# Optimization experiments

Measured on AMD Instinct MI355X. Metric: run time of the kernel, lower is better.

The kernel has to match this reference:

```python
import jax, jax.numpy as jnp
import numpy as np

B, T, D, H = 256, 1024, 128, 128

def setup_inputs() -> dict:
    key = jax.random.key(0)
    k1, k2, k3, k4 = jax.random.split(key, 4)
    return {
        "x": jax.random.normal(k1, (B, T, D), dtype=jnp.float32),
        "w": jax.random.normal(k2, (D, H), dtype=jnp.float32) * 0.05,
        "state_weight": jax.random.normal(k3, (H, H), dtype=jnp.float32) * 0.05,
        "b": jax.random.normal(k4, (H,), dtype=jnp.float32) * 0.05,
    }

def reference(x, w, state_weight, b):
    # Faithful Elman RNN with return_sequences=False.
    # Original transposes input to time-major [T, B, D], initializes the
    # state from step 0 WITHOUT a recurrent term, then iterates steps 1..T-1.
    X = jnp.transpose(x, (1, 0, 2))  # [T, B, D]
    # Precompute input projections for all steps in one big GEMM (same math).
    proj = jnp.einsum("tbd,dh->tbh", X, w) + b  # [T, B, H]
    state0 = jnp.tanh(proj[0])

    def step(state, pt):
        y = jnp.tanh(pt + state @ state_weight)
        return y, None

    final_state, _ = jax.lax.scan(step, state0, proj[1:])
    return final_state  # [B, H]
```

## Files before the change

kernel.cpp:

```cpp
#include <hip/hip_runtime.h>

#define T_N 1024
#define H_N 128
#define CH   64
#define NCH (T_N / CH)
#define WPAD 136
#define PPAD 68
#define XGRP 1040
#define XBUF_BYTES (32 * XGRP)

typedef __attribute__((ext_vector_type(8))) short bf16x8;
typedef __attribute__((ext_vector_type(4))) float f32x4;

__device__ __forceinline__ short f2bf_rne(float f) {
    union { float f; unsigned int i; } v; v.f = f;
    unsigned int r = v.i + 0x7FFFu + ((v.i >> 16) & 1u);
    return (short)(r >> 16);
}
__device__ __forceinline__ float tanh_fast(float x) {
    return 1.0f - 2.0f / (__expf(2.0f * x) + 1.0f);
}

__global__ __launch_bounds__(256, 1) void k_fused(const float* __restrict__ x,
                                                  const float* __restrict__ w,
                                                  const float* __restrict__ wst,
                                                  const float* __restrict__ bias,
                                                  float* __restrict__ out) {
    __shared__ __align__(16) short wT[H_N * WPAD];
    __shared__ __align__(16) float pT[H_N * PPAD];
    __shared__ __align__(16) char  xbuf[2][XBUF_BYTES];
    __shared__ __align__(16) short sst[2][H_N];

    const int tid  = threadIdx.x;
    const int wv   = tid >> 6;
    const int lane = tid & 63;
    const int l = lane & 15;
    const int q = lane >> 4;
    const int r = blockIdx.x;
    const float* xrow = x + (size_t)r * T_N * H_N;
    const f32x4 zero4 = (f32x4){0.f, 0.f, 0.f, 0.f};

    {
        const char* gsrc = (const char*)xrow;
        #pragma unroll
        for (int kk = 0; kk < 8; ++kk) {
            int k = wv * 8 + kk;
            __builtin_amdgcn_global_load_lds(
                (const __attribute__((address_space(1))) void*)(gsrc + k * 1024 + lane * 16),
                (__attribute__((address_space(3))) void*)(&xbuf[0][k * XGRP]),
                16, 0, 0);
        }
    }

    short* wsT = reinterpret_cast<short*>(pT);
    for (int e = tid * 4; e < H_N * H_N; e += 1024) {
        int k = e >> 7, n = e & 127;
        float4 a4 = *reinterpret_cast<const float4*>(wst + e);
        wsT[(n + 0) * WPAD + k] = f2bf_rne(a4.x);
        wsT[(n + 1) * WPAD + k] = f2bf_rne(a4.y);
        wsT[(n + 2) * WPAD + k] = f2bf_rne(a4.z);
        wsT[(n + 3) * WPAD + k] = f2bf_rne(a4.w);
    }
    __syncthreads();

    bf16x8 wf[2][4];
    #pragma unroll
    for (int b = 0; b < 2; ++b)
        #pragma unroll
        for (int ks = 0; ks < 4; ++ks)
            wf[b][ks] = *reinterpret_cast<const bf16x8*>(
                &wsT[(16 * (2 * wv + b) + l) * WPAD + ks * 32 + q * 8]);

    for (int e = tid * 4; e < H_N * H_N; e += 1024) {
        int k = e >> 7, n = e & 127;
        float4 a4 = *reinterpret_cast<const float4*>(w + e);
        wT[(n + 0) * WPAD + k] = f2bf_rne(a4.x);
        wT[(n + 1) * WPAD + k] = f2bf_rne(a4.y);
        wT[(n + 2) * WPAD + k] = f2bf_rne(a4.z);
        wT[(n + 3) * WPAD + k] = f2bf_rne(a4.w);
    }

    float bv[8];
    #pragma unroll
    for (int nt = 0; nt < 8; ++nt) bv[nt] = bias[nt * 16 + l];

    int par = 0;
    float y0 = 0.f, y1 = 0.f;

    #pragma unroll 1
    for (int c = 0; c < NCH; ++c) {
        __syncthreads();

        {
            const char* xb = xbuf[c & 1];
            int row = wv * 16 + l;
            const float* pr = reinterpret_cast<const float*>(
                xb + (row >> 1) * XGRP + (row & 1) * 512);
            bf16x8 ax[4];
            #pragma unroll
            for (int ks = 0; ks < 4; ++ks) {
                float4 u0 = *reinterpret_cast<const float4*>(pr + ks * 32 + q * 8);
                float4 u1 = *reinterpret_cast<const float4*>(pr + ks * 32 + q * 8 + 4);
                bf16x8 f;
                f[0] = f2bf_rne(u0.x); f[1] = f2bf_rne(u0.y);
                f[2] = f2bf_rne(u0.z); f[3] = f2bf_rne(u0.w);
                f[4] = f2bf_rne(u1.x); f[5] = f2bf_rne(u1.y);
                f[6] = f2bf_rne(u1.z); f[7] = f2bf_rne(u1.w);
                ax[ks] = f;
            }
            #pragma unroll
            for (int nt = 0; nt < 8; ++nt) {
                f32x4 acc;
                #pragma unroll
                for (int ks = 0; ks < 4; ++ks) {
                    bf16x8 bw = *reinterpret_cast<const bf16x8*>(
                        &wT[(nt * 16 + l) * WPAD + ks * 32 + q * 8]);
                    acc = __builtin_amdgcn_mfma_f32_16x16x32_bf16(
                        ax[ks], bw, ks == 0 ? zero4 : acc, 0, 0, 0);
                }
                f32x4 o = (f32x4){acc[0] + bv[nt], acc[1] + bv[nt],
                                  acc[2] + bv[nt], acc[3] + bv[nt]};
                *reinterpret_cast<f32x4*>(&pT[(nt * 16 + l) * PPAD + wv * 16 + q * 4]) = o;
            }
        }

        if (c + 1 < NCH) {
            const char* gsrc = (const char*)(xrow + (size_t)(c + 1) * CH * H_N);
            char* ldst = &xbuf[(c + 1) & 1][0];
            #pragma unroll
            for (int kk = 0; kk < 8; ++kk) {
                int k = wv * 8 + kk;
                __builtin_amdgcn_global_load_lds(
                    (const __attribute__((address_space(1))) void*)(gsrc + k * 1024 + lane * 16),
                    (__attribute__((address_space(3))) void*)(ldst + k * XGRP),
                    16, 0, 0);
            }
        }

        __syncthreads();

        int tstart = 0;
        if (c == 0) {
            if (tid < 128) sst[0][tid] = f2bf_rne(tanh_fast(pT[tid * PPAD + 0]));
            __syncthreads();
            tstart = 1;
            par = 0;
        }

        float p0 = pT[(32 * wv + l) * PPAD + tstart];
        float p1 = pT[(32 * wv + 16 + l) * PPAD + tstart];

        #pragma unroll 1
        for (int t = tstart; t < CH; ++t) {
            bf16x8 a[4];
            #pragma unroll
            for (int ks = 0; ks < 4; ++ks)
                a[ks] = *reinterpret_cast<const bf16x8*>(&sst[par][ks * 32 + q * 8]);

            f32x4 acc[8];
            #pragma unroll
            for (int ks = 0; ks < 4; ++ks) {
                acc[ks]     = __builtin_amdgcn_mfma_f32_16x16x32_bf16(a[ks], wf[0][ks], zero4, 0, 0, 0);
                acc[4 + ks] = __builtin_amdgcn_mfma_f32_16x16x32_bf16(a[ks], wf[1][ks], zero4, 0, 0, 0);
            }

            int tn = (t + 1 < CH) ? t + 1 : t;
            float np0 = pT[(32 * wv + l) * PPAD + tn];
            float np1 = pT[(32 * wv + 16 + l) * PPAD + tn];

            float z0 = p0 + ((acc[0][0] + acc[1][0]) + (acc[2][0] + acc[3][0]));
            float z1 = p1 + ((acc[4][0] + acc[5][0]) + (acc[6][0] + acc[7][0]));
            y0 = tanh_fast(z0);
            y1 = tanh_fast(z1);
            sst[par ^ 1][32 * wv + l]      = f2bf_rne(y0);
            sst[par ^ 1][32 * wv + 16 + l] = f2bf_rne(y1);
            p0 = np0; p1 = np1;
            par ^= 1;
            __syncthreads();
        }
    }

    if (q == 0) {
        out[r * H_N + 32 * wv + l]      = y0;
        out[r * H_N + 32 * wv + 16 + l] = y1;
    }
}

extern "C" void kernel_launch(void* const* d_in, const int* in_sizes, int n_in,
                              void* d_out, int out_size, void* d_ws, size_t ws_size,
                              hipStream_t stream) {
    const float* x    = (const float*)d_in[0];
    const float* w    = (const float*)d_in[1];
    const float* wst  = (const float*)d_in[2];
    const float* bias = (const float*)d_in[3];
    float* out = (float*)d_out;

    k_fused<<<256, 256, 0, stream>>>(x, w, wst, bias, out);
}
```

Baseline: 464.4 us.

## Double chunk size, keep input weights in registers, pack state stores with permuted layout

Raises the time chunk from 64 to 128 steps and drops x double-buffering. The next chunk's x is now loaded into a single buffer after the projection finishes reading it, which halves the number of chunk transitions. The input projection weights are loaded once into registers, so each wave computes its own 32 output columns for all rows and the per-chunk LDS weight reads go away. The recurrent state is written as one packed 32-bit store per lane, using a permuted slot layout matched in the recurrent weights. Per-step __syncthreads are replaced with an lgkmcnt wait plus s_barrier. The risk is that x-load latency is no longer hidden behind the recurrence at chunk boundaries.

```diff
diff --git a/kernel.cpp b/kernel.cpp
--- a/kernel.cpp
+++ b/kernel.cpp
@@ -2,15 +2,16 @@
 
 #define T_N 1024
 #define H_N 128
-#define CH   64
+#define CH   128
 #define NCH (T_N / CH)
-#define WPAD 136
-#define PPAD 68
+#define SPAD 136
+#define PPAD 132
 #define XGRP 1040
-#define XBUF_BYTES (32 * XGRP)
 
 typedef __attribute__((ext_vector_type(8))) short bf16x8;
 typedef __attribute__((ext_vector_type(4))) float f32x4;
+
+#define BAR_LGKM() asm volatile("s_waitcnt lgkmcnt(0)\n\ts_barrier" ::: "memory")
 
 __device__ __forceinline__ short f2bf_rne(float f) {
     union { float f; unsigned int i; } v; v.f = f;
@@ -19,6 +20,9 @@
 }
 __device__ __forceinline__ float tanh_fast(float x) {
     return 1.0f - 2.0f / (__expf(2.0f * x) + 1.0f);
+}
+__device__ __forceinline__ int slotof(int c) {
+    return (c & 0x60) | ((c & 0x0F) << 1) | ((c >> 4) & 1);
 }
 
 __global__ __launch_bounds__(256, 1) void k_fused(const float* __restrict__ x,
@@ -26,9 +30,8 @@
                                                   const float* __restrict__ wst,
                                                   const float* __restrict__ bias,
                                                   float* __restrict__ out) {
-    __shared__ __align__(16) short wT[H_N * WPAD];
     __shared__ __align__(16) float pT[H_N * PPAD];
-    __shared__ __align__(16) char  xbuf[2][XBUF_BYTES];
+    __shared__ __align__(16) char  xbuf[64 * XGRP];
     __shared__ __align__(16) short sst[2][H_N];
 
     const int tid  = threadIdx.x;
@@ -43,46 +46,54 @@
     {
         const char* gsrc = (const char*)xrow;
         #pragma unroll
-        for (int kk = 0; kk < 8; ++kk) {
-            int k = wv * 8 + kk;
+        for (int kk = 0; kk < 16; ++kk) {
+            int k = wv * 16 + kk;
             __builtin_amdgcn_global_load_lds(
                 (const __attribute__((address_space(1))) void*)(gsrc + k * 1024 + lane * 16),
-                (__attribute__((address_space(3))) void*)(&xbuf[0][k * XGRP]),
+                (__attribute__((address_space(3))) void*)(&xbuf[k * XGRP]),
                 16, 0, 0);
         }
     }
 
-    short* wsT = reinterpret_cast<short*>(pT);
+    short* stg = reinterpret_cast<short*>(pT);
+
     for (int e = tid * 4; e < H_N * H_N; e += 1024) {
-        int k = e >> 7, n = e & 127;
+        int k = e >> 7, n = e & 127, s = slotof(k);
         float4 a4 = *reinterpret_cast<const float4*>(wst + e);
-        wsT[(n + 0) * WPAD + k] = f2bf_rne(a4.x);
-        wsT[(n + 1) * WPAD + k] = f2bf_rne(a4.y);
-        wsT[(n + 2) * WPAD + k] = f2bf_rne(a4.z);
-        wsT[(n + 3) * WPAD + k] = f2bf_rne(a4.w);
-    }
-    __syncthreads();
-
+        stg[(n + 0) * SPAD + s] = f2bf_rne(a4.x);
+        stg[(n + 1) * SPAD + s] = f2bf_rne(a4.y);
+        stg[(n + 2) * SPAD + s] = f2bf_rne(a4.z);
+        stg[(n + 3) * SPAD + s] = f2bf_rne(a4.w);
+    }
+    __syncthreads();
     bf16x8 wf[2][4];
     #pragma unroll
     for (int b = 0; b < 2; ++b)
         #pragma unroll
         for (int ks = 0; ks < 4; ++ks)
             wf[b][ks] = *reinterpret_cast<const bf16x8*>(
-                &wsT[(16 * (2 * wv + b) + l) * WPAD + ks * 32 + q * 8]);
+                &stg[(16 * (2 * wv + b) + l) * SPAD + ks * 32 + q * 8]);
+    __syncthreads();
 
     for (int e = tid * 4; e < H_N * H_N; e += 1024) {
         int k = e >> 7, n = e & 127;
         float4 a4 = *reinterpret_cast<const float4*>(w + e);
-        wT[(n + 0) * WPAD + k] = f2bf_rne(a4.x);
-        wT[(n + 1) * WPAD + k] = f2bf_rne(a4.y);
-        wT[(n + 2) * WPAD + k] = f2bf_rne(a4.z);
-        wT[(n + 3) * WPAD + k] = f2bf_rne(a4.w);
-    }
-
-    float bv[8];
+        stg[(n + 0) * SPAD + k] = f2bf_rne(a4.x);
+        stg[(n + 1) * SPAD + k] = f2bf_rne(a4.y);
+        stg[(n + 2) * SPAD + k] = f2bf_rne(a4.z);
+        stg[(n + 3) * SPAD + k] = f2bf_rne(a4.w);
+    }
+    __syncthreads();
+    bf16x8 wfin[2][4];
     #pragma unroll
-    for (int nt = 0; nt < 8; ++nt) bv[nt] = bias[nt * 16 + l];
+    for (int b = 0; b < 2; ++b)
+        #pragma unroll
+        for (int ks = 0; ks < 4; ++ks)
+            wfin[b][ks] = *reinterpret_cast<const bf16x8*>(
+                &stg[(16 * (2 * wv + b) + l) * SPAD + ks * 32 + q * 8]);
+    float bv0 = bias[16 * (2 * wv + 0) + l];
+    float bv1 = bias[16 * (2 * wv + 1) + l];
+    __syncthreads();
 
     int par = 0;
     float y0 = 0.f, y1 = 0.f;
@@ -91,11 +102,11 @@
     for (int c = 0; c < NCH; ++c) {
         __syncthreads();
 
-        {
-            const char* xb = xbuf[c & 1];
-            int row = wv * 16 + l;
+        #pragma unroll
+        for (int rt = 0; rt < 8; ++rt) {
+            int row = rt * 16 + l;
             const float* pr = reinterpret_cast<const float*>(
-                xb + (row >> 1) * XGRP + (row & 1) * 512);
+                xbuf + (row >> 1) * XGRP + (row & 1) * 512);
             bf16x8 ax[4];
             #pragma unroll
             for (int ks = 0; ks < 4; ++ks) {
@@ -109,40 +120,37 @@
                 ax[ks] = f;
             }
             #pragma unroll
-            for (int nt = 0; nt < 8; ++nt) {
+            for (int b = 0; b < 2; ++b) {
                 f32x4 acc;
                 #pragma unroll
-                for (int ks = 0; ks < 4; ++ks) {
-                    bf16x8 bw = *reinterpret_cast<const bf16x8*>(
-                        &wT[(nt * 16 + l) * WPAD + ks * 32 + q * 8]);
+                for (int ks = 0; ks < 4; ++ks)
                     acc = __builtin_amdgcn_mfma_f32_16x16x32_bf16(
-                        ax[ks], bw, ks == 0 ? zero4 : acc, 0, 0, 0);
-                }
-                f32x4 o = (f32x4){acc[0] + bv[nt], acc[1] + bv[nt],
-                                  acc[2] + bv[nt], acc[3] + bv[nt]};
-                *reinterpret_cast<f32x4*>(&pT[(nt * 16 + l) * PPAD + wv * 16 + q * 4]) = o;
-            }
-        }
+                        ax[ks], wfin[b][ks], ks == 0 ? zero4 : acc, 0, 0, 0);
+                float bb = b ? bv1 : bv0;
+                f32x4 o = (f32x4){acc[0] + bb, acc[1] + bb, acc[2] + bb, acc[3] + bb};
+                *reinterpret_cast<f32x4*>(
+                    &pT[(16 * (2 * wv + b) + l) * PPAD + rt * 16 + q * 4]) = o;
+            }
+        }
+        BAR_LGKM();
 
         if (c + 1 < NCH) {
             const char* gsrc = (const char*)(xrow + (size_t)(c + 1) * CH * H_N);
-            char* ldst = &xbuf[(c + 1) & 1][0];
-            #pragma unroll
-            for (int kk = 0; kk < 8; ++kk) {
-                int k = wv * 8 + kk;
+            #pragma unroll
+            for (int kk = 0; kk < 16; ++kk) {
+                int k = wv * 16 + kk;
                 __builtin_amdgcn_global_load_lds(
                     (const __attribute__((address_space(1))) void*)(gsrc + k * 1024 + lane * 16),
-                    (__attribute__((address_space(3))) void*)(ldst + k * XGRP),
+                    (__attribute__((address_space(3))) void*)(&xbuf[k * XGRP]),
                     16, 0, 0);
             }
         }
-
-        __syncthreads();
 
         int tstart = 0;
         if (c == 0) {
-            if (tid < 128) sst[0][tid] = f2bf_rne(tanh_fast(pT[tid * PPAD + 0]));
-            __syncthreads();
+            if (tid < 128)
+                sst[0][slotof(tid)] = f2bf_rne(tanh_fast(pT[tid * PPAD]));
+            BAR_LGKM();
             tstart = 1;
             par = 0;
         }
@@ -172,11 +180,15 @@
             float z1 = p1 + ((acc[4][0] + acc[5][0]) + (acc[6][0] + acc[7][0]));
             y0 = tanh_fast(z0);
             y1 = tanh_fast(z1);
-            sst[par ^ 1][32 * wv + l]      = f2bf_rne(y0);
-            sst[par ^ 1][32 * wv + 16 + l] = f2bf_rne(y1);
+
+            if (q == 0) {
+                unsigned int pk = (unsigned int)(unsigned short)f2bf_rne(y0)
+                                | ((unsigned int)(unsigned short)f2bf_rne(y1) << 16);
+                *reinterpret_cast<unsigned int*>(&sst[par ^ 1][32 * wv + 2 * l]) = pk;
+            }
             p0 = np0; p1 = np1;
             par ^= 1;
-            __syncthreads();
+            BAR_LGKM();
         }
     }
 
```

Measured after the change: 518.2 us. 11.6% more time.

## Unroll recurrence by four with vector pT loads and lighter LDS-only barriers

Applied to the files above, without the earlier changes.

Replaces __syncthreads in the serial recurrence with a custom s_waitcnt lgkmcnt(0) + s_barrier, so the barrier no longer waits on outstanding global/vmem loads. The per-chunk x prefetch is issued before the projection GEMM, which lets it overlap that compute and the recurrence. The time loop is unrolled by 4 with float4 loads of precomputed projections, reducing per-step LDS reads and loop overhead. Not waiting on vmcnt is intended to let the async global_load_lds stay in flight, and an extra sync is added after reading the state weights. The risk is an ordering hazard on the LDS buffer that the async loads write into.

```diff
diff --git a/kernel.cpp b/kernel.cpp
--- a/kernel.cpp
+++ b/kernel.cpp
@@ -11,6 +11,8 @@
 
 typedef __attribute__((ext_vector_type(8))) short bf16x8;
 typedef __attribute__((ext_vector_type(4))) float f32x4;
+
+#define BAR_LGKM() asm volatile("s_waitcnt lgkmcnt(0)\n\ts_barrier" ::: "memory")
 
 __device__ __forceinline__ short f2bf_rne(float f) {
     union { float f; unsigned int i; } v; v.f = f;
@@ -70,6 +72,7 @@
         for (int ks = 0; ks < 4; ++ks)
             wf[b][ks] = *reinterpret_cast<const bf16x8*>(
                 &wsT[(16 * (2 * wv + b) + l) * WPAD + ks * 32 + q * 8]);
+    __syncthreads();
 
     for (int e = tid * 4; e < H_N * H_N; e += 1024) {
         int k = e >> 7, n = e & 127;
@@ -86,10 +89,25 @@
 
     int par = 0;
     float y0 = 0.f, y1 = 0.f;
+    const int row0 = (32 * wv + l) * PPAD;
+    const int row1 = (32 * wv + 16 + l) * PPAD;
 
     #pragma unroll 1
     for (int c = 0; c < NCH; ++c) {
         __syncthreads();
+
+        if (c + 1 < NCH) {
+            const char* gsrc = (const char*)(xrow + (size_t)(c + 1) * CH * H_N);
+            char* ldst = &xbuf[(c + 1) & 1][0];
+            #pragma unroll
+            for (int kk = 0; kk < 8; ++kk) {
+                int k = wv * 8 + kk;
+                __builtin_amdgcn_global_load_lds(
+                    (const __attribute__((address_space(1))) void*)(gsrc + k * 1024 + lane * 16),
+                    (__attribute__((address_space(3))) void*)(ldst + k * XGRP),
+                    16, 0, 0);
+            }
+        }
 
         {
             const char* xb = xbuf[c & 1];
@@ -123,60 +141,50 @@
                 *reinterpret_cast<f32x4*>(&pT[(nt * 16 + l) * PPAD + wv * 16 + q * 4]) = o;
             }
         }
-
-        if (c + 1 < NCH) {
-            const char* gsrc = (const char*)(xrow + (size_t)(c + 1) * CH * H_N);
-            char* ldst = &xbuf[(c + 1) & 1][0];
-            #pragma unroll
-            for (int kk = 0; kk < 8; ++kk) {
-                int k = wv * 8 + kk;
-                __builtin_amdgcn_global_load_lds(
-                    (const __attribute__((address_space(1))) void*)(gsrc + k * 1024 + lane * 16),
-                    (__attribute__((address_space(3))) void*)(ldst + k * XGRP),
-                    16, 0, 0);
-            }
-        }
-
-        __syncthreads();
-
-        int tstart = 0;
+        BAR_LGKM();
+
         if (c == 0) {
-            if (tid < 128) sst[0][tid] = f2bf_rne(tanh_fast(pT[tid * PPAD + 0]));
-            __syncthreads();
-            tstart = 1;
+            if (tid < 128)
+                sst[0][tid] = f2bf_rne(tanh_fast(pT[tid * PPAD + 0]));
+            BAR_LGKM();
             par = 0;
         }
 
-        float p0 = pT[(32 * wv + l) * PPAD + tstart];
-        float p1 = pT[(32 * wv + 16 + l) * PPAD + tstart];
+        float4 pc0 = *reinterpret_cast<const float4*>(&pT[row0]);
+        float4 pc1 = *reinterpret_cast<const float4*>(&pT[row1]);
 
         #pragma unroll 1
-        for (int t = tstart; t < CH; ++t) {
-            bf16x8 a[4];
-            #pragma unroll
-            for (int ks = 0; ks < 4; ++ks)
-                a[ks] = *reinterpret_cast<const bf16x8*>(&sst[par][ks * 32 + q * 8]);
-
-            f32x4 acc[8];
-            #pragma unroll
-            for (int ks = 0; ks < 4; ++ks) {
-                acc[ks]     = __builtin_amdgcn_mfma_f32_16x16x32_bf16(a[ks], wf[0][ks], zero4, 0, 0, 0);
-                acc[4 + ks] = __builtin_amdgcn_mfma_f32_16x16x32_bf16(a[ks], wf[1][ks], zero4, 0, 0, 0);
-            }
-
-            int tn = (t + 1 < CH) ? t + 1 : t;
-            float np0 = pT[(32 * wv + l) * PPAD + tn];
-            float np1 = pT[(32 * wv + 16 + l) * PPAD + tn];
-
-            float z0 = p0 + ((acc[0][0] + acc[1][0]) + (acc[2][0] + acc[3][0]));
-            float z1 = p1 + ((acc[4][0] + acc[5][0]) + (acc[6][0] + acc[7][0]));
-            y0 = tanh_fast(z0);
-            y1 = tanh_fast(z1);
-            sst[par ^ 1][32 * wv + l]      = f2bf_rne(y0);
-            sst[par ^ 1][32 * wv + 16 + l] = f2bf_rne(y1);
-            p0 = np0; p1 = np1;
-            par ^= 1;
-            __syncthreads();
+        for (int t4 = 0; t4 < CH / 4; ++t4) {
+            int t4n = (t4 + 1 < CH / 4) ? t4 + 1 : t4;
+            float4 nx0 = *reinterpret_cast<const float4*>(&pT[row0 + t4n * 4]);
+            float4 nx1 = *reinterpret_cast<const float4*>(&pT[row1 + t4n * 4]);
+
+            #pragma unroll
+            for (int u = 0; u < 4; ++u) {
+                if (c == 0 && t4 == 0 && u == 0) continue;
+
+                bf16x8 a[4];
+                #pragma unroll
+                for (int ks = 0; ks < 4; ++ks)
+                    a[ks] = *reinterpret_cast<const bf16x8*>(&sst[par][ks * 32 + q * 8]);
+
+                f32x4 acc[8];
+                #pragma unroll
+                for (int ks = 0; ks < 4; ++ks) {
+                    acc[ks]     = __builtin_amdgcn_mfma_f32_16x16x32_bf16(a[ks], wf[0][ks], zero4, 0, 0, 0);
+                    acc[4 + ks] = __builtin_amdgcn_mfma_f32_16x16x32_bf16(a[ks], wf[1][ks], zero4, 0, 0, 0);
+                }
+
+                float z0 = pc0[u] + ((acc[0][0] + acc[1][0]) + (acc[2][0] + acc[3][0]));
+                float z1 = pc1[u] + ((acc[4][0] + acc[5][0]) + (acc[6][0] + acc[7][0]));
+                y0 = tanh_fast(z0);
+                y1 = tanh_fast(z1);
+                sst[par ^ 1][32 * wv + l]      = f2bf_rne(y0);
+                sst[par ^ 1][32 * wv + 16 + l] = f2bf_rne(y1);
+                par ^= 1;
+                BAR_LGKM();
+            }
+            pc0 = nx0; pc1 = nx1;
         }
     }
 
```

Result: slower. 486.1 us (+4.7%).

## Permute recurrent state layout for packed stores, fold bias into MFMA, lighten barriers

Applied to the files above, without the earlier changes.

Reorders the K dimension of the recurrent weight and the state vector with a slot permutation. Each lane can then write y0 and y1 as one packed 32-bit LDS store, and only q==0 lanes store. The per-step projection is injected as the MFMA accumulator init instead of being added afterwards. __syncthreads is replaced by an inline-asm lgkmcnt wait plus s_barrier that does not wait on vmcnt, so the in-flight global_load_lds prefetch is not drained each step. The asm barrier may let the prefetched x buffer be read before its async load completes, because there is no vmcnt wait before the chunk compute.

```diff
diff --git a/kernel.cpp b/kernel.cpp
--- a/kernel.cpp
+++ b/kernel.cpp
@@ -12,6 +12,8 @@
 typedef __attribute__((ext_vector_type(8))) short bf16x8;
 typedef __attribute__((ext_vector_type(4))) float f32x4;
 
+#define BAR_LGKM() asm volatile("s_waitcnt lgkmcnt(0)\n\ts_barrier" ::: "memory")
+
 __device__ __forceinline__ short f2bf_rne(float f) {
     union { float f; unsigned int i; } v; v.f = f;
     unsigned int r = v.i + 0x7FFFu + ((v.i >> 16) & 1u);
@@ -19,6 +21,9 @@
 }
 __device__ __forceinline__ float tanh_fast(float x) {
     return 1.0f - 2.0f / (__expf(2.0f * x) + 1.0f);
+}
+__device__ __forceinline__ int slotof(int c) {
+    return (c & 0x60) | ((c & 0x0F) << 1) | ((c >> 4) & 1);
 }
 
 __global__ __launch_bounds__(256, 1) void k_fused(const float* __restrict__ x,
@@ -54,12 +59,12 @@
 
     short* wsT = reinterpret_cast<short*>(pT);
     for (int e = tid * 4; e < H_N * H_N; e += 1024) {
-        int k = e >> 7, n = e & 127;
+        int k = e >> 7, n = e & 127, s = slotof(k);
         float4 a4 = *reinterpret_cast<const float4*>(wst + e);
-        wsT[(n + 0) * WPAD + k] = f2bf_rne(a4.x);
-        wsT[(n + 1) * WPAD + k] = f2bf_rne(a4.y);
-        wsT[(n + 2) * WPAD + k] = f2bf_rne(a4.z);
-        wsT[(n + 3) * WPAD + k] = f2bf_rne(a4.w);
+        wsT[(n + 0) * WPAD + s] = f2bf_rne(a4.x);
+        wsT[(n + 1) * WPAD + s] = f2bf_rne(a4.y);
+        wsT[(n + 2) * WPAD + s] = f2bf_rne(a4.z);
+        wsT[(n + 3) * WPAD + s] = f2bf_rne(a4.w);
     }
     __syncthreads();
 
@@ -70,6 +75,7 @@
         for (int ks = 0; ks < 4; ++ks)
             wf[b][ks] = *reinterpret_cast<const bf16x8*>(
                 &wsT[(16 * (2 * wv + b) + l) * WPAD + ks * 32 + q * 8]);
+    __syncthreads();
 
     for (int e = tid * 4; e < H_N * H_N; e += 1024) {
         int k = e >> 7, n = e & 127;
@@ -86,6 +92,8 @@
 
     int par = 0;
     float y0 = 0.f, y1 = 0.f;
+    const int row0 = (32 * wv + l) * PPAD;
+    const int row1 = (32 * wv + 16 + l) * PPAD;
 
     #pragma unroll 1
     for (int c = 0; c < NCH; ++c) {
@@ -132,23 +140,25 @@
                 int k = wv * 8 + kk;
                 __builtin_amdgcn_global_load_lds(
                     (const __attribute__((address_space(1))) void*)(gsrc + k * 1024 + lane * 16),
-                    (__attribute__((address_space(3))) void*)(ldst + k * XGRP),
+                    (__attribute__((address_space(3))) void*)(&xbuf[(c + 1) & 1][k * XGRP]),
                     16, 0, 0);
             }
-        }
-
-        __syncthreads();
+            (void)ldst;
+        }
+
+        BAR_LGKM();
 
         int tstart = 0;
         if (c == 0) {
-            if (tid < 128) sst[0][tid] = f2bf_rne(tanh_fast(pT[tid * PPAD + 0]));
-            __syncthreads();
+            if (tid < 128)
+                sst[0][slotof(tid)] = f2bf_rne(tanh_fast(pT[tid * PPAD + 0]));
+            BAR_LGKM();
             tstart = 1;
             par = 0;
         }
 
-        float p0 = pT[(32 * wv + l) * PPAD + tstart];
-        float p1 = pT[(32 * wv + 16 + l) * PPAD + tstart];
+        float p0 = pT[row0 + tstart];
+        float p1 = pT[row1 + tstart];
 
         #pragma unroll 1
         for (int t = tstart; t < CH; ++t) {
@@ -157,26 +167,34 @@
             for (int ks = 0; ks < 4; ++ks)
                 a[ks] = *reinterpret_cast<const bf16x8*>(&sst[par][ks * 32 + q * 8]);
 
+            f32x4 c0 = (f32x4){p0, 0.f, 0.f, 0.f};
+            f32x4 c1 = (f32x4){p1, 0.f, 0.f, 0.f};
             f32x4 acc[8];
             #pragma unroll
             for (int ks = 0; ks < 4; ++ks) {
-                acc[ks]     = __builtin_amdgcn_mfma_f32_16x16x32_bf16(a[ks], wf[0][ks], zero4, 0, 0, 0);
-                acc[4 + ks] = __builtin_amdgcn_mfma_f32_16x16x32_bf16(a[ks], wf[1][ks], zero4, 0, 0, 0);
+                acc[ks]     = __builtin_amdgcn_mfma_f32_16x16x32_bf16(
+                                  a[ks], wf[0][ks], ks == 0 ? c0 : zero4, 0, 0, 0);
+                acc[4 + ks] = __builtin_amdgcn_mfma_f32_16x16x32_bf16(
+                                  a[ks], wf[1][ks], ks == 0 ? c1 : zero4, 0, 0, 0);
             }
 
             int tn = (t + 1 < CH) ? t + 1 : t;
-            float np0 = pT[(32 * wv + l) * PPAD + tn];
-            float np1 = pT[(32 * wv + 16 + l) * PPAD + tn];
-
-            float z0 = p0 + ((acc[0][0] + acc[1][0]) + (acc[2][0] + acc[3][0]));
-            float z1 = p1 + ((acc[4][0] + acc[5][0]) + (acc[6][0] + acc[7][0]));
+            float np0 = pT[row0 + tn];
+            float np1 = pT[row1 + tn];
+
+            float z0 = (acc[0][0] + acc[1][0]) + (acc[2][0] + acc[3][0]);
+            float z1 = (acc[4][0] + acc[5][0]) + (acc[6][0] + acc[7][0]);
             y0 = tanh_fast(z0);
             y1 = tanh_fast(z1);
-            sst[par ^ 1][32 * wv + l]      = f2bf_rne(y0);
-            sst[par ^ 1][32 * wv + 16 + l] = f2bf_rne(y1);
+
+            if (q == 0) {
+                unsigned int pk = (unsigned int)(unsigned short)f2bf_rne(y0)
+                                | ((unsigned int)(unsigned short)f2bf_rne(y1) << 16);
+                *reinterpret_cast<unsigned int*>(&sst[par ^ 1][32 * wv + 2 * l]) = pk;
+            }
             p0 = np0; p1 = np1;
             par ^= 1;
-            __syncthreads();
+            BAR_LGKM();
         }
     }
 
```

Result: slower. 518.2 us (+11.6%).
